# Optimization experiments

Hardware: AMD Instinct MI355X
Metric: run time of the kernel (lower is better)

Reference implementation:

```python
import jax, jax.numpy as jnp
import numpy as np

NUM_TOKENS = 8192
MODEL_DIM = 4096
NUM_EXPERTS = 64
CAPACITY_FACTOR = 1.0


def setup_inputs() -> dict:
    key = jax.random.key(0)
    k1, k2 = jax.random.split(key)
    inp = jax.random.normal(k1, (NUM_TOKENS, MODEL_DIM), dtype=jnp.float32)
    wg = jax.random.normal(k2, (NUM_EXPERTS, MODEL_DIM), dtype=jnp.float32) * (1.0 / np.sqrt(MODEL_DIM))
    return {"input": inp, "wg_weight": wg}


def reference(input, wg_weight):
    # logits = input @ wg.T  -> [T, E]
    logits = jnp.einsum('td,ed->te', input, wg_weight)
    num_tokens, num_experts = logits.shape
    capacity = int(CAPACITY_FACTOR * ((num_tokens + num_experts - 1) // num_experts))

    indices1_s = jnp.argmax(logits, axis=1)                      # [T]
    mask1 = jax.nn.one_hot(indices1_s, num_experts, dtype=logits.dtype)  # [T, E]
    gates = jax.nn.softmax(logits, axis=1)                       # [T, E]
    gates1_s = jnp.sum(gates * mask1, axis=1)                    # [T]

    # locations: position of each token within its chosen expert's queue
    # (exclusive cumsum over the one-hot mask, gathered at the chosen expert)
    locations1 = jnp.cumsum(mask1, axis=0) - 1.0                 # [T, E]
    locations1_s = jnp.sum(locations1 * mask1, axis=1).astype(jnp.int32)  # [T]

    # load-balancing aux loss (float32 branch of the original)
    me = jnp.sum(gates, axis=0)                                  # [E]
    ce = jnp.sum(mask1, axis=0)                                  # [E]
    l_aux = jnp.sum(me * ce) * (num_experts / (num_tokens * num_tokens))

    return (l_aux, indices1_s.astype(jnp.int32), locations1_s, gates1_s)
```

## Files before the change

kernel.cpp:

```cpp
#include <hip/hip_runtime.h>

namespace {
constexpr int TOK = 8192;
constexpr int DIM = 4096;
constexpr int NE  = 64;
constexpr int TB  = 128;
constexpr int KS  = 4;
constexpr int KR  = DIM / KS;
constexpr int NKS = KR / 32;
constexpr int NRND = NKS / 8;
constexpr int NT  = TOK / TB;
constexpr int GB  = 64;
constexpr int NCH = TOK / GB;
}

typedef _Float16 f16x8 __attribute__((ext_vector_type(8)));
typedef float    f32x4 __attribute__((ext_vector_type(4)));

__global__ __launch_bounds__(512, 4) void gemm_split(
    const float* __restrict__ A, const float* __restrict__ W,
    float* __restrict__ partial) {
  __shared__ _Float16 sB[8 * 8 * 64 * 8];

  const int bid  = blockIdx.x;
  const int tile = bid & (NT - 1);
  const int ks   = bid / NT;
  const int t0   = tile * TB;
  const int tid  = threadIdx.x;
  const int w    = tid >> 6;
  const int lane = tid & 63;
  const int col  = lane & 15;
  const int quad = lane >> 4;

  const int etw = w & 3;
  const int s0  = (w >> 2) * 4;
  const float* Wp = W + (size_t)(etw * 16 + col) * DIM + ks * KR + quad * 8;

  const float* Ap = A + (size_t)(t0 + w * 16 + col) * DIM + ks * KR + quad * 8;

  f32x4 acc[4];
#pragma unroll
  for (int et = 0; et < 4; ++et) acc[et] = (f32x4)0.0f;

  float4 a0  = *(const float4*)(Ap);
  float4 a1  = *(const float4*)(Ap + 4);
  float4 a0n = *(const float4*)(Ap + 32);
  float4 a1n = *(const float4*)(Ap + 36);

  for (int rnd = 0; rnd < NRND; ++rnd) {
    if (rnd) __syncthreads();
#pragma unroll
    for (int s = s0; s < s0 + 4; ++s) {
      const float4 w0 = *(const float4*)(Wp + (rnd * 8 + s) * 32);
      const float4 w1 = *(const float4*)(Wp + (rnd * 8 + s) * 32 + 4);
      const float wv[8] = {w0.x, w0.y, w0.z, w0.w, w1.x, w1.y, w1.z, w1.w};
      f16x8 hi, lo;
#pragma unroll
      for (int j = 0; j < 8; ++j) {
        const _Float16 h = (_Float16)wv[j];
        hi[j] = h;
        lo[j] = (_Float16)(wv[j] - (float)h);
      }
      *(f16x8*)(sB + ((etw * 8 + s) << 9) + lane * 8) = hi;
      *(f16x8*)(sB + (((4 + etw) * 8 + s) << 9) + lane * 8) = lo;
    }
    __syncthreads();

    for (int s = 0; s < 8; ++s) {
      const int it = rnd * 8 + s;
      float4 a0nn, a1nn;
      if (it + 2 < NKS) {
        a0nn = *(const float4*)(Ap + (it + 2) * 32);
        a1nn = *(const float4*)(Ap + (it + 2) * 32 + 4);
      }
      const float av[8] = {a0.x, a0.y, a0.z, a0.w, a1.x, a1.y, a1.z, a1.w};
      f16x8 ah, al;
#pragma unroll
      for (int j = 0; j < 8; ++j) {
        const _Float16 h = (_Float16)av[j];
        ah[j] = h;
        al[j] = (_Float16)(av[j] - (float)h);
      }
#pragma unroll
      for (int et = 0; et < 4; ++et) {
        const f16x8 bh = *(const f16x8*)(sB + ((et * 8 + s) << 9) + lane * 8);
        const f16x8 bl =
            *(const f16x8*)(sB + (((4 + et) * 8 + s) << 9) + lane * 8);
        acc[et] = __builtin_amdgcn_mfma_f32_16x16x32_f16(ah, bh, acc[et], 0, 0, 0);
        acc[et] = __builtin_amdgcn_mfma_f32_16x16x32_f16(ah, bl, acc[et], 0, 0, 0);
        acc[et] = __builtin_amdgcn_mfma_f32_16x16x32_f16(al, bh, acc[et], 0, 0, 0);
      }
      a0 = a0n; a1 = a1n; a0n = a0nn; a1n = a1nn;
    }
  }

  float* P = partial + (size_t)ks * TOK * NE;
  const int tb = t0 + w * 16 + quad * 4;
#pragma unroll
  for (int et = 0; et < 4; ++et) {
    const int e = et * 16 + col;
#pragma unroll
    for (int r = 0; r < 4; ++r)
      P[(size_t)(tb + r) * NE + e] = acc[et][r];
  }
}

__global__ __launch_bounds__(256) void gating(
    const float* __restrict__ partial, float* __restrict__ out,
    int* __restrict__ idx_int, int* __restrict__ rankp,
    int* __restrict__ hist, float* __restrict__ me_part) {
  __shared__ float L[GB * 65];
  __shared__ float pm[4][GB];
  __shared__ int   pi[4][GB];
  __shared__ float ps[4][GB];
  __shared__ float mep[4][NE];
  __shared__ float mx[GB];
  __shared__ float dninv[GB];
  __shared__ int   eid[GB];
  const int b = blockIdx.x, tid = threadIdx.x;
  const int t = tid & 63, q = tid >> 6;
  const size_t base = (size_t)b * GB * NE;

#pragma unroll
  for (int j = 0; j < 4; ++j) {
    const int i4 = tid + 256 * j;
    const int tt = i4 >> 4, e4 = (i4 & 15) * 4;
    f32x4 s = (f32x4)0.0f;
#pragma unroll
    for (int k = 0; k < KS; ++k) {
      const f32x4 v = *(const f32x4*)(partial + (size_t)k * TOK * NE + base +
                                      (size_t)tt * NE + e4);
      s += v;
    }
    *(f32x4*)(L + tt * 65 + e4) = s;
  }
  __syncthreads();

  {
    float m = -3.0e38f; int bi = q * 16;
#pragma unroll
    for (int e = q * 16; e < q * 16 + 16; ++e) {
      const float v = L[t * 65 + e];
      if (v > m) { m = v; bi = e; }
    }
    pm[q][t] = m; pi[q][t] = bi;
  }
  __syncthreads();
  if (tid < GB) {
    float m = -3.0e38f; int bi = 0;
#pragma unroll
    for (int qq = 0; qq < 4; ++qq) {
      if (pm[qq][tid] > m) { m = pm[qq][tid]; bi = pi[qq][tid]; }
    }
    mx[tid] = m; eid[tid] = bi;
    const int gt = b * GB + tid;
    out[1 + gt] = (float)bi;
    idx_int[gt] = bi;
  }
  __syncthreads();
  {
    const float m = mx[t];
    float s = 0.0f;
#pragma unroll
    for (int e = q * 16; e < q * 16 + 16; ++e) s += __expf(L[t * 65 + e] - m);
    ps[q][t] = s;
  }
  __syncthreads();
  if (tid < GB) {
    const float inv = 1.0f / (ps[0][tid] + ps[1][tid] + ps[2][tid] + ps[3][tid]);
    dninv[tid] = inv;
    out[1 + 2 * TOK + b * GB + tid] = inv;
  }
  __syncthreads();
  {
    const int e = t;
    float s = 0.0f;
#pragma unroll
    for (int tt = q * 16; tt < q * 16 + 16; ++tt)
      s += __expf(L[tt * 65 + e] - mx[tt]) * dninv[tt];
    mep[q][e] = s;
  }
  __syncthreads();
  if (tid < GB) {
    const int e = eid[tid];
    int r = 0;
    for (int j = 0; j < tid; ++j) r += (eid[j] == e) ? 1 : 0;
    rankp[b * GB + tid] = r;
    int c = 0;
    for (int t2 = 0; t2 < GB; ++t2) c += (eid[t2] == tid) ? 1 : 0;
    hist[b * NE + tid] = c;
  } else if (tid < 2 * GB) {
    const int e = tid - GB;
    me_part[b * NE + e] = mep[0][e] + mep[1][e] + mep[2][e] + mep[3][e];
  }
}

__global__ __launch_bounds__(1024) void finalize(
    const int* __restrict__ idx_int, const int* __restrict__ rankp,
    const int* __restrict__ hist, const float* __restrict__ me_part,
    float* __restrict__ out) {
  __shared__ int   H[NCH * NE];
  __shared__ int   SEG[16 * NE];
  __shared__ float MEp[16 * NE];
  __shared__ float CE[NE];
  const int tid = threadIdx.x;
  const int e = tid & 63, seg = tid >> 6;

  for (int j = tid; j < NCH * NE; j += 1024) H[j] = hist[j];
  {
    float s = 0.0f;
    for (int c = seg * 8; c < seg * 8 + 8; ++c) s += me_part[c * NE + e];
    MEp[seg * NE + e] = s;
  }
  __syncthreads();
  {
    int hs = 0;
    for (int c = seg * 8; c < seg * 8 + 8; ++c) hs += H[c * NE + e];
    SEG[seg * NE + e] = hs;
  }
  __syncthreads();
  if (tid < NE) {
    int run = 0;
    for (int s2 = 0; s2 < 16; ++s2) {
      const int v = SEG[s2 * NE + tid];
      SEG[s2 * NE + tid] = run;
      run += v;
    }
    CE[tid] = (float)run;
  }
  __syncthreads();
  {
    int run = SEG[seg * NE + e];
    for (int c = seg * 8; c < seg * 8 + 8; ++c) {
      const int v = H[c * NE + e];
      H[c * NE + e] = run;
      run += v;
    }
  }
  if (tid < 64) {
    float me = 0.0f;
#pragma unroll
    for (int s2 = 0; s2 < 16; ++s2) me += MEp[s2 * NE + tid];
    float p = me * CE[tid];
#pragma unroll
    for (int off = 32; off > 0; off >>= 1) p += __shfl_down(p, off);
    if (tid == 0) out[0] = p * ((float)NE / ((float)TOK * (float)TOK));
  }
  __syncthreads();
#pragma unroll
  for (int i = tid; i < TOK; i += 1024) {
    const int ex = idx_int[i];
    out[1 + TOK + i] = (float)(H[(i >> 6) * NE + ex] + rankp[i]);
  }
}

extern "C" void kernel_launch(void* const* d_in, const int* in_sizes, int n_in,
                              void* d_out, int out_size, void* d_ws, size_t ws_size,
                              hipStream_t stream) {
  const float* A = (const float*)d_in[0];
  const float* W = (const float*)d_in[1];
  float* out = (float*)d_out;
  char* ws = (char*)d_ws;

  float* partial = (float*)ws;
  size_t off = (size_t)KS * TOK * NE * sizeof(float);
  float* me_part = (float*)(ws + off);  off += (size_t)NCH * NE * sizeof(float);
  int* idx_int = (int*)(ws + off);      off += (size_t)TOK * sizeof(int);
  int* rankp   = (int*)(ws + off);      off += (size_t)TOK * sizeof(int);
  int* hist    = (int*)(ws + off);

  hipLaunchKernelGGL(gemm_split, dim3(NT * KS), dim3(512), 0, stream,
                     A, W, partial);
  hipLaunchKernelGGL(gating, dim3(NCH), dim3(256), 0, stream, partial, out,
                     idx_int, rankp, hist, me_part);
  hipLaunchKernelGGL(finalize, dim3(1), dim3(1024), 0, stream, idx_int, rankp,
                     hist, me_part, out);
}
```

Before: 218.8 us.

## Fuse gate GEMM with gating epilogue, drop split-K and shared-memory W staging

```diff
diff --git a/kernel.cpp b/kernel.cpp
--- a/kernel.cpp
+++ b/kernel.cpp
@@ -4,194 +4,147 @@
 constexpr int TOK = 8192;
 constexpr int DIM = 4096;
 constexpr int NE  = 64;
-constexpr int TB  = 128;
-constexpr int KS  = 4;
-constexpr int KR  = DIM / KS;
-constexpr int NKS = KR / 32;
-constexpr int NRND = NKS / 8;
-constexpr int NT  = TOK / TB;
-constexpr int GB  = 64;
-constexpr int NCH = TOK / GB;
+constexpr int TB  = 32;
+constexpr int NB  = TOK / TB;
+constexpr int NK  = DIM / 32;
 }
 
 typedef _Float16 f16x8 __attribute__((ext_vector_type(8)));
 typedef float    f32x4 __attribute__((ext_vector_type(4)));
 
-__global__ __launch_bounds__(512, 4) void gemm_split(
+__global__ __launch_bounds__(512) void gemm_gate(
     const float* __restrict__ A, const float* __restrict__ W,
-    float* __restrict__ partial) {
-  __shared__ _Float16 sB[8 * 8 * 64 * 8];
-
-  const int bid  = blockIdx.x;
-  const int tile = bid & (NT - 1);
-  const int ks   = bid / NT;
-  const int t0   = tile * TB;
+    float* __restrict__ out, int* __restrict__ idx_int,
+    int* __restrict__ rankp, int* __restrict__ hist,
+    float* __restrict__ me_part) {
+  __shared__ float L[TB * 65];
+  __shared__ float pm[8][TB];
+  __shared__ int   pi[8][TB];
+  __shared__ float ps[8][TB];
+  __shared__ float mep[8][NE];
+  __shared__ float mx[TB];
+  __shared__ float dninv[TB];
+  __shared__ int   eid[TB];
+
+  const int b    = blockIdx.x;
   const int tid  = threadIdx.x;
   const int w    = tid >> 6;
   const int lane = tid & 63;
   const int col  = lane & 15;
   const int quad = lane >> 4;
-
-  const int etw = w & 3;
-  const int s0  = (w >> 2) * 4;
-  const float* Wp = W + (size_t)(etw * 16 + col) * DIM + ks * KR + quad * 8;
-
-  const float* Ap = A + (size_t)(t0 + w * 16 + col) * DIM + ks * KR + quad * 8;
-
-  f32x4 acc[4];
-#pragma unroll
-  for (int et = 0; et < 4; ++et) acc[et] = (f32x4)0.0f;
+  const int mt   = w & 1;
+  const int et   = w >> 1;
+
+  const float* Ap = A + (size_t)(b * TB + mt * 16 + col) * DIM + quad * 8;
+  const float* Wp = W + (size_t)(et * 16 + col) * DIM + quad * 8;
+
+  f32x4 acc = (f32x4)0.0f;
 
   float4 a0  = *(const float4*)(Ap);
   float4 a1  = *(const float4*)(Ap + 4);
+  float4 w0  = *(const float4*)(Wp);
+  float4 w1  = *(const float4*)(Wp + 4);
   float4 a0n = *(const float4*)(Ap + 32);
   float4 a1n = *(const float4*)(Ap + 36);
-
-  for (int rnd = 0; rnd < NRND; ++rnd) {
-    if (rnd) __syncthreads();
-#pragma unroll
-    for (int s = s0; s < s0 + 4; ++s) {
-      const float4 w0 = *(const float4*)(Wp + (rnd * 8 + s) * 32);
-      const float4 w1 = *(const float4*)(Wp + (rnd * 8 + s) * 32 + 4);
-      const float wv[8] = {w0.x, w0.y, w0.z, w0.w, w1.x, w1.y, w1.z, w1.w};
-      f16x8 hi, lo;
-#pragma unroll
-      for (int j = 0; j < 8; ++j) {
-        const _Float16 h = (_Float16)wv[j];
-        hi[j] = h;
-        lo[j] = (_Float16)(wv[j] - (float)h);
-      }
-      *(f16x8*)(sB + ((etw * 8 + s) << 9) + lane * 8) = hi;
-      *(f16x8*)(sB + (((4 + etw) * 8 + s) << 9) + lane * 8) = lo;
-    }
-    __syncthreads();
-
-    for (int s = 0; s < 8; ++s) {
-      const int it = rnd * 8 + s;
-      float4 a0nn, a1nn;
-      if (it + 2 < NKS) {
-        a0nn = *(const float4*)(Ap + (it + 2) * 32);
-        a1nn = *(const float4*)(Ap + (it + 2) * 32 + 4);
-      }
-      const float av[8] = {a0.x, a0.y, a0.z, a0.w, a1.x, a1.y, a1.z, a1.w};
-      f16x8 ah, al;
-#pragma unroll
-      for (int j = 0; j < 8; ++j) {
-        const _Float16 h = (_Float16)av[j];
-        ah[j] = h;
-        al[j] = (_Float16)(av[j] - (float)h);
-      }
-#pragma unroll
-      for (int et = 0; et < 4; ++et) {
-        const f16x8 bh = *(const f16x8*)(sB + ((et * 8 + s) << 9) + lane * 8);
-        const f16x8 bl =
-            *(const f16x8*)(sB + (((4 + et) * 8 + s) << 9) + lane * 8);
-        acc[et] = __builtin_amdgcn_mfma_f32_16x16x32_f16(ah, bh, acc[et], 0, 0, 0);
-        acc[et] = __builtin_amdgcn_mfma_f32_16x16x32_f16(ah, bl, acc[et], 0, 0, 0);
-        acc[et] = __builtin_amdgcn_mfma_f32_16x16x32_f16(al, bh, acc[et], 0, 0, 0);
-      }
-      a0 = a0n; a1 = a1n; a0n = a0nn; a1n = a1nn;
-    }
-  }
-
-  float* P = partial + (size_t)ks * TOK * NE;
-  const int tb = t0 + w * 16 + quad * 4;
-#pragma unroll
-  for (int et = 0; et < 4; ++et) {
-    const int e = et * 16 + col;
-#pragma unroll
-    for (int r = 0; r < 4; ++r)
-      P[(size_t)(tb + r) * NE + e] = acc[et][r];
-  }
-}
-
-__global__ __launch_bounds__(256) void gating(
-    const float* __restrict__ partial, float* __restrict__ out,
-    int* __restrict__ idx_int, int* __restrict__ rankp,
-    int* __restrict__ hist, float* __restrict__ me_part) {
-  __shared__ float L[GB * 65];
-  __shared__ float pm[4][GB];
-  __shared__ int   pi[4][GB];
-  __shared__ float ps[4][GB];
-  __shared__ float mep[4][NE];
-  __shared__ float mx[GB];
-  __shared__ float dninv[GB];
-  __shared__ int   eid[GB];
-  const int b = blockIdx.x, tid = threadIdx.x;
-  const int t = tid & 63, q = tid >> 6;
-  const size_t base = (size_t)b * GB * NE;
-
-#pragma unroll
-  for (int j = 0; j < 4; ++j) {
-    const int i4 = tid + 256 * j;
-    const int tt = i4 >> 4, e4 = (i4 & 15) * 4;
-    f32x4 s = (f32x4)0.0f;
-#pragma unroll
-    for (int k = 0; k < KS; ++k) {
-      const f32x4 v = *(const f32x4*)(partial + (size_t)k * TOK * NE + base +
-                                      (size_t)tt * NE + e4);
-      s += v;
-    }
-    *(f32x4*)(L + tt * 65 + e4) = s;
-  }
-  __syncthreads();
-
-  {
-    float m = -3.0e38f; int bi = q * 16;
-#pragma unroll
-    for (int e = q * 16; e < q * 16 + 16; ++e) {
+  float4 w0n = *(const float4*)(Wp + 32);
+  float4 w1n = *(const float4*)(Wp + 36);
+
+  for (int it = 0; it < NK; ++it) {
+    float4 a0nn, a1nn, w0nn, w1nn;
+    if (it + 2 < NK) {
+      a0nn = *(const float4*)(Ap + (it + 2) * 32);
+      a1nn = *(const float4*)(Ap + (it + 2) * 32 + 4);
+      w0nn = *(const float4*)(Wp + (it + 2) * 32);
+      w1nn = *(const float4*)(Wp + (it + 2) * 32 + 4);
+    }
+    const float av[8] = {a0.x, a0.y, a0.z, a0.w, a1.x, a1.y, a1.z, a1.w};
+    const float wv[8] = {w0.x, w0.y, w0.z, w0.w, w1.x, w1.y, w1.z, w1.w};
+    f16x8 ah, al, wh, wl;
+#pragma unroll
+    for (int j = 0; j < 8; ++j) {
+      const _Float16 h = (_Float16)av[j];
+      ah[j] = h;
+      al[j] = (_Float16)(av[j] - (float)h);
+      const _Float16 g = (_Float16)wv[j];
+      wh[j] = g;
+      wl[j] = (_Float16)(wv[j] - (float)g);
+    }
+    acc = __builtin_amdgcn_mfma_f32_16x16x32_f16(ah, wh, acc, 0, 0, 0);
+    acc = __builtin_amdgcn_mfma_f32_16x16x32_f16(ah, wl, acc, 0, 0, 0);
+    acc = __builtin_amdgcn_mfma_f32_16x16x32_f16(al, wh, acc, 0, 0, 0);
+    a0 = a0n; a1 = a1n; w0 = w0n; w1 = w1n;
+    a0n = a0nn; a1n = a1nn; w0n = w0nn; w1n = w1nn;
+  }
+
+#pragma unroll
+  for (int r = 0; r < 4; ++r)
+    L[(mt * 16 + quad * 4 + r) * 65 + et * 16 + col] = acc[r];
+  __syncthreads();
+
+  const int t = tid & 31, q = tid >> 5;
+  if (tid < 256) {
+    float m = -3.0e38f; int bi = q * 8;
+#pragma unroll
+    for (int e = q * 8; e < q * 8 + 8; ++e) {
       const float v = L[t * 65 + e];
       if (v > m) { m = v; bi = e; }
     }
     pm[q][t] = m; pi[q][t] = bi;
   }
   __syncthreads();
-  if (tid < GB) {
+  if (tid < TB) {
     float m = -3.0e38f; int bi = 0;
 #pragma unroll
-    for (int qq = 0; qq < 4; ++qq) {
+    for (int qq = 0; qq < 8; ++qq)
       if (pm[qq][tid] > m) { m = pm[qq][tid]; bi = pi[qq][tid]; }
-    }
     mx[tid] = m; eid[tid] = bi;
-    const int gt = b * GB + tid;
+    const int gt = b * TB + tid;
     out[1 + gt] = (float)bi;
     idx_int[gt] = bi;
   }
   __syncthreads();
-  {
+  if (tid < 256) {
     const float m = mx[t];
     float s = 0.0f;
 #pragma unroll
-    for (int e = q * 16; e < q * 16 + 16; ++e) s += __expf(L[t * 65 + e] - m);
+    for (int e = q * 8; e < q * 8 + 8; ++e) s += __expf(L[t * 65 + e] - m);
     ps[q][t] = s;
   }
   __syncthreads();
-  if (tid < GB) {
-    const float inv = 1.0f / (ps[0][tid] + ps[1][tid] + ps[2][tid] + ps[3][tid]);
+  if (tid < TB) {
+    float s = 0.0f;
+#pragma unroll
+    for (int qq = 0; qq < 8; ++qq) s += ps[qq][tid];
+    const float inv = 1.0f / s;
     dninv[tid] = inv;
-    out[1 + 2 * TOK + b * GB + tid] = inv;
-  }
-  __syncthreads();
-  {
-    const int e = t;
-    float s = 0.0f;
-#pragma unroll
-    for (int tt = q * 16; tt < q * 16 + 16; ++tt)
+    out[1 + 2 * TOK + b * TB + tid] = inv;
+  }
+  __syncthreads();
+  {
+    const int e = tid & 63, g = tid >> 6;
+    float s = 0.0f;
+#pragma unroll
+    for (int tt = g * 4; tt < g * 4 + 4; ++tt)
       s += __expf(L[tt * 65 + e] - mx[tt]) * dninv[tt];
-    mep[q][e] = s;
-  }
-  __syncthreads();
-  if (tid < GB) {
+    mep[g][e] = s;
+  }
+  __syncthreads();
+  if (tid < TB) {
     const int e = eid[tid];
     int r = 0;
     for (int j = 0; j < tid; ++j) r += (eid[j] == e) ? 1 : 0;
-    rankp[b * GB + tid] = r;
+    rankp[b * TB + tid] = r;
+  } else if (tid >= 64 && tid < 128) {
+    const int e = tid - 64;
     int c = 0;
-    for (int t2 = 0; t2 < GB; ++t2) c += (eid[t2] == tid) ? 1 : 0;
-    hist[b * NE + tid] = c;
-  } else if (tid < 2 * GB) {
-    const int e = tid - GB;
-    me_part[b * NE + e] = mep[0][e] + mep[1][e] + mep[2][e] + mep[3][e];
+    for (int t2 = 0; t2 < TB; ++t2) c += (eid[t2] == e) ? 1 : 0;
+    hist[b * NE + e] = c;
+  } else if (tid >= 128 && tid < 192) {
+    const int e = tid - 128;
+    float s = 0.0f;
+#pragma unroll
+    for (int g = 0; g < 8; ++g) s += mep[g][e];
+    me_part[b * NE + e] = s;
   }
 }
 
@@ -199,23 +152,23 @@
     const int* __restrict__ idx_int, const int* __restrict__ rankp,
     const int* __restrict__ hist, const float* __restrict__ me_part,
     float* __restrict__ out) {
-  __shared__ int   H[NCH * NE];
+  __shared__ int   H[NB * NE];
   __shared__ int   SEG[16 * NE];
   __shared__ float MEp[16 * NE];
   __shared__ float CE[NE];
   const int tid = threadIdx.x;
   const int e = tid & 63, seg = tid >> 6;
 
-  for (int j = tid; j < NCH * NE; j += 1024) H[j] = hist[j];
-  {
-    float s = 0.0f;
-    for (int c = seg * 8; c < seg * 8 + 8; ++c) s += me_part[c * NE + e];
+  for (int j = tid; j < NB * NE; j += 1024) H[j] = hist[j];
+  {
+    float s = 0.0f;
+    for (int c = seg * 16; c < seg * 16 + 16; ++c) s += me_part[c * NE + e];
     MEp[seg * NE + e] = s;
   }
   __syncthreads();
   {
     int hs = 0;
-    for (int c = seg * 8; c < seg * 8 + 8; ++c) hs += H[c * NE + e];
+    for (int c = seg * 16; c < seg * 16 + 16; ++c) hs += H[c * NE + e];
     SEG[seg * NE + e] = hs;
   }
   __syncthreads();
@@ -231,7 +184,7 @@
   __syncthreads();
   {
     int run = SEG[seg * NE + e];
-    for (int c = seg * 8; c < seg * 8 + 8; ++c) {
+    for (int c = seg * 16; c < seg * 16 + 16; ++c) {
       const int v = H[c * NE + e];
       H[c * NE + e] = run;
       run += v;
@@ -250,7 +203,7 @@
 #pragma unroll
   for (int i = tid; i < TOK; i += 1024) {
     const int ex = idx_int[i];
-    out[1 + TOK + i] = (float)(H[(i >> 6) * NE + ex] + rankp[i]);
+    out[1 + TOK + i] = (float)(H[(i >> 5) * NE + ex] + rankp[i]);
   }
 }
 
@@ -262,17 +215,14 @@
   float* out = (float*)d_out;
   char* ws = (char*)d_ws;
 
-  float* partial = (float*)ws;
-  size_t off = (size_t)KS * TOK * NE * sizeof(float);
-  float* me_part = (float*)(ws + off);  off += (size_t)NCH * NE * sizeof(float);
+  size_t off = 0;
+  float* me_part = (float*)(ws + off);  off += (size_t)NB * NE * sizeof(float);
   int* idx_int = (int*)(ws + off);      off += (size_t)TOK * sizeof(int);
   int* rankp   = (int*)(ws + off);      off += (size_t)TOK * sizeof(int);
   int* hist    = (int*)(ws + off);
 
-  hipLaunchKernelGGL(gemm_split, dim3(NT * KS), dim3(512), 0, stream,
-                     A, W, partial);
-  hipLaunchKernelGGL(gating, dim3(NCH), dim3(256), 0, stream, partial, out,
-                     idx_int, rankp, hist, me_part);
+  hipLaunchKernelGGL(gemm_gate, dim3(NB), dim3(512), 0, stream,
+                     A, W, out, idx_int, rankp, hist, me_part);
   hipLaunchKernelGGL(finalize, dim3(1), dim3(1024), 0, stream, idx_int, rankp,
                      hist, me_part, out);
 }
```

Result: slower. 270.3 us (+23.5%).
